# Performance work log

Measured on AMD Instinct MI355X. Metric: run time of the kernel, lower is better.

## Reference

```python
import jax, jax.numpy as jnp
import numpy as np

BN_EPS = 1e-5

def _conv1x1(x, w, b):
    # x: [B,C,H,W], w: [O,C], b: [O] -> [B,O,H,W]
    return jnp.einsum('bchw,oc->bohw', x, w) + b[None, :, None, None]

def setup_inputs() -> dict:
    key = jax.random.key(0)
    ks = jax.random.split(key, 9)
    B, C, H, W = 8, 256, 64, 64
    I = C // 2
    s_in = 1.0 / np.sqrt(C)
    s_out = 1.0 / np.sqrt(I)
    return {
        'x':       jax.random.normal(ks[0], (B, C, H, W), dtype=jnp.float32),
        'g_w':     jax.random.uniform(ks[1], (I, C), jnp.float32, -s_in, s_in),
        'g_b':     jax.random.uniform(ks[2], (I,),  jnp.float32, -s_in, s_in),
        'theta_w': jax.random.uniform(ks[3], (I, C), jnp.float32, -s_in, s_in),
        'theta_b': jax.random.uniform(ks[4], (I,),  jnp.float32, -s_in, s_in),
        'phi_w':   jax.random.uniform(ks[5], (I, C), jnp.float32, -s_in, s_in),
        'phi_b':   jax.random.uniform(ks[6], (I,),  jnp.float32, -s_in, s_in),
        'w_w':     jax.random.uniform(ks[7], (C, I), jnp.float32, -s_out, s_out),
        'w_b':     jax.random.uniform(ks[8], (C,),  jnp.float32, -s_out, s_out),
        'gamma':   jnp.ones((C,), dtype=jnp.float32),   # BN weight init constant 1
        'beta':    jnp.zeros((C,), dtype=jnp.float32),  # BN bias init constant 0
    }

def reference(x, g_w, g_b, theta_w, theta_b, phi_w, phi_b, w_w, w_b, gamma, beta):
    B, C, H, W = x.shape
    I = g_w.shape[0]
    N = H * W
    g_x     = _conv1x1(x, g_w, g_b).reshape(B, I, N)          # [B,I,N]
    theta_x = _conv1x1(x, theta_w, theta_b).reshape(B, I, N)  # [B,I,N]
    phi_x   = _conv1x1(x, phi_w, phi_b).reshape(B, I, N)      # [B,I,N]
    # f = theta^T @ phi : [B,N,N]
    f = jnp.einsum('bin,bim->bnm', theta_x, phi_x)
    a = jax.nn.softmax(f, axis=-1)
    # y = a @ g^T : [B,N,I] -> [B,I,H,W]
    y = jnp.einsum('bnm,bim->bin', a, g_x).reshape(B, I, H, W)
    wy = _conv1x1(y, w_w, w_b)                                # [B,C,H,W]
    # BatchNorm2d (training mode: batch statistics over B,H,W per channel)
    mean = jnp.mean(wy, axis=(0, 2, 3), keepdims=True)
    var = jnp.var(wy, axis=(0, 2, 3), keepdims=True)
    wy_bn = (wy - mean) * jax.lax.rsqrt(var + BN_EPS)
    wy_bn = wy_bn * gamma[None, :, None, None] + beta[None, :, None, None]
    return wy_bn + x
```

## Files before the change

kernel.cpp:

```cpp
#include <hip/hip_runtime.h>

#define B_ 8
#define C_ 256
#define I_ 128
#define N_ 4096
#define BN_ (B_ * N_)
#define LOG2E 1.4426950408889634f

typedef __attribute__((ext_vector_type(8))) short bf16x8;
typedef __attribute__((ext_vector_type(4))) float f32x4;
typedef __attribute__((ext_vector_type(4))) int i32x4;

static __device__ __forceinline__ short f2bf(float f) {
    unsigned u = __float_as_uint(f);
    unsigned r = u + 0x7fffu + ((u >> 16) & 1u);
    return (short)(r >> 16);
}
static __device__ __forceinline__ float bf2f(short s) {
    return __uint_as_float(((unsigned)(unsigned short)s) << 16);
}
static __device__ __forceinline__ unsigned cvt_pk_bf16(float lo, float hi) {
    unsigned r;
    asm("v_cvt_pk_bf16_f32 %0, %1, %2" : "=v"(r) : "v"(lo), "v"(hi));
    return r;
}

__global__ void k_prep(const float* g_w, const float* theta_w, const float* phi_w,
                       const float* g_b, const float* theta_b, const float* phi_b,
                       const float* w_w, short* wcat, short* wwb, float* bcat) {
    int i = blockIdx.x * 256 + threadIdx.x;
    if (i < 384 * 256) {
        int j = i >> 8, c = i & 255;
        float v = (j < 128) ? theta_w[j * 256 + c] * LOG2E
                : (j < 256) ? phi_w[(j - 128) * 256 + c]
                            : g_w[(j - 256) * 256 + c];
        wcat[i] = f2bf(v);
    } else if (i < 384 * 256 + 256 * 128) {
        int k = i - 384 * 256;
        wwb[k] = f2bf(w_w[k]);
    } else if (i < 384 * 256 + 256 * 128 + 384) {
        int j = i - (384 * 256 + 256 * 128);
        bcat[j] = (j < 128) ? theta_b[j] * LOG2E
                : (j < 256) ? phi_b[j - 128] : g_b[j - 256];
    }
}

__global__ __launch_bounds__(256) void k_proj(const float* __restrict__ x,
                                              const short* __restrict__ wcat,
                                              const float* __restrict__ bcat,
                                              short* __restrict__ tp,
                                              short* __restrict__ gmat) {
    int b = blockIdx.y;
    int n0 = blockIdx.x * 64;
    int tid = threadIdx.x;
    int wave = tid >> 6, lane = tid & 63, s = lane & 15, q = lane >> 4;
    __shared__ short xs[64][264];

#pragma unroll
    for (int it = 0; it < 16; ++it) {
        int cr = (tid >> 4) + it * 16;
        int nc = tid & 15;
        const float4 v = *(const float4*)&x[((size_t)b * C_ + cr) * N_ + n0 + nc * 4];
        xs[nc * 4 + 0][cr] = f2bf(v.x);
        xs[nc * 4 + 1][cr] = f2bf(v.y);
        xs[nc * 4 + 2][cr] = f2bf(v.z);
        xs[nc * 4 + 3][cr] = f2bf(v.w);
    }
    __syncthreads();

    f32x4 acc[4][6];
#pragma unroll
    for (int rt = 0; rt < 4; ++rt)
#pragma unroll
        for (int jt = 0; jt < 6; ++jt) acc[rt][jt] = (f32x4){0.f, 0.f, 0.f, 0.f};

#pragma unroll
    for (int kb = 0; kb < 8; ++kb) {
        bf16x8 af[4], bfv[6];
#pragma unroll
        for (int rt = 0; rt < 4; ++rt)
            af[rt] = *(const bf16x8*)&xs[rt * 16 + s][kb * 32 + q * 8];
#pragma unroll
        for (int jt = 0; jt < 6; ++jt)
            bfv[jt] = *(const bf16x8*)&wcat[(wave * 96 + jt * 16 + s) * 256 + kb * 32 + q * 8];
#pragma unroll
        for (int rt = 0; rt < 4; ++rt)
#pragma unroll
            for (int jt = 0; jt < 6; ++jt)
                acc[rt][jt] = __builtin_amdgcn_mfma_f32_16x16x32_bf16(af[rt], bfv[jt], acc[rt][jt], 0, 0, 0);
    }

#pragma unroll
    for (int rt = 0; rt < 4; ++rt)
#pragma unroll
        for (int jt = 0; jt < 6; ++jt) {
            int j = wave * 96 + jt * 16 + s;
            float bias = bcat[j];
#pragma unroll
            for (int r = 0; r < 4; ++r) {
                int n = n0 + rt * 16 + 4 * q + r;
                float v = acc[rt][jt][r] + bias;
                if (j < 256)
                    tp[((size_t)b * N_ + n) * 256 + j] = f2bf(v);
                else
                    gmat[((size_t)b * I_ + (j - 256)) * N_ + n] = f2bf(v);
            }
        }
}

__global__ __launch_bounds__(512, 2) void k_attn_wy(const short* __restrict__ tp,
                                                    const short* __restrict__ gmat,
                                                    const short* __restrict__ wwb,
                                                    const float* __restrict__ w_b,
                                                    short* __restrict__ wyh) {
    int id = blockIdx.x;
    int b = id & 7;
    int qt = id >> 3;
    int n0 = qt * 128;
    int tid = threadIdx.x;
    int wave = tid >> 6, lane = tid & 63, s = lane & 15, q = lane >> 4;

    __shared__ __align__(16) short SH[65536];
    __shared__ float l_lds[128];
    char* base = (char*)SH;

    const int swz = (s & 7) << 4;
    int kA[4];
#pragma unroll
    for (int kb = 0; kb < 4; ++kb) kA[kb] = s * 256 + ((kb * 64 + q * 16) ^ swz);
    int vA[2];
#pragma unroll
    for (int kb2 = 0; kb2 < 2; ++kb2) vA[kb2] = s * 256 + ((kb2 * 64 + q * 16) ^ swz);
    int krow = tid >> 4, kch = tid & 15;
    int stW = krow * 256 + ((kch * 16) ^ ((krow & 7) << 4));

    bf16x8 qf[4];
    {
        const short* qb = tp + ((size_t)b * N_ + n0 + wave * 16 + s) * 256;
#pragma unroll
        for (int kb = 0; kb < 4; ++kb) qf[kb] = *(const bf16x8*)(qb + kb * 32 + q * 8);
    }

    f32x4 ot[8];
#pragma unroll
    for (int t = 0; t < 8; ++t) ot[t] = (f32x4){0.f, 0.f, 0.f, 0.f};
    float lsum = 0.f;

    bf16x8 pk[4], pv[4];
#pragma unroll
    for (int it = 0; it < 4; ++it) {
        pk[it] = *(const bf16x8*)&tp[((size_t)b * N_ + krow + it * 32) * 256 + 128 + kch * 8];
        pv[it] = *(const bf16x8*)&gmat[((size_t)b * I_ + krow + it * 32) * N_ + kch * 8];
    }
#pragma unroll
    for (int it = 0; it < 4; ++it) {
        *(bf16x8*)(base + stW + it * 8192) = pk[it];
        *(bf16x8*)(base + 32768 + stW + it * 8192) = pv[it];
    }
    __syncthreads();

    for (int i = 0; i < 32; ++i) {
        char* KtB = base + (i & 1) * 65536;
        char* VtB = KtB + 32768;
        if (i < 31) {
            int m = (i + 1) * 128;
#pragma unroll
            for (int it = 0; it < 4; ++it) {
                pk[it] = *(const bf16x8*)&tp[((size_t)b * N_ + m + krow + it * 32) * 256 + 128 + kch * 8];
                pv[it] = *(const bf16x8*)&gmat[((size_t)b * I_ + krow + it * 32) * N_ + m + kch * 8];
            }
        }

#pragma unroll
        for (int h = 0; h < 2; ++h) {
            const int hK = h * 16384, hV = h * 128;

            f32x4 sa[4];
#pragma unroll
            for (int tc = 0; tc < 4; ++tc) sa[tc] = (f32x4){0.f, 0.f, 0.f, 0.f};
            __builtin_amdgcn_s_setprio(1);
#pragma unroll
            for (int tc = 0; tc < 4; ++tc) {
#pragma unroll
                for (int kb = 0; kb < 4; ++kb) {
                    bf16x8 bfv = *(const bf16x8*)(KtB + hK + kA[kb] + tc * 4096);
                    sa[tc] = __builtin_amdgcn_mfma_f32_16x16x32_bf16(bfv, qf[kb], sa[tc], 0, 0, 0);
                }
            }
            __builtin_amdgcn_s_setprio(0);

#pragma unroll
            for (int tc = 0; tc < 4; ++tc)
#pragma unroll
                for (int r = 0; r < 4; ++r) sa[tc][r] = exp2f(sa[tc][r]);
            {
                float t0 = (sa[0][0] + sa[0][1]) + (sa[0][2] + sa[0][3]);
                float t1 = (sa[1][0] + sa[1][1]) + (sa[1][2] + sa[1][3]);
                float t2 = (sa[2][0] + sa[2][1]) + (sa[2][2] + sa[2][3]);
                float t3 = (sa[3][0] + sa[3][1]) + (sa[3][2] + sa[3][3]);
                lsum += (t0 + t1) + (t2 + t3);
            }
            unsigned W[4][2];
#pragma unroll
            for (int tc = 0; tc < 4; ++tc) {
                W[tc][0] = cvt_pk_bf16(sa[tc][0], sa[tc][1]);
                W[tc][1] = cvt_pk_bf16(sa[tc][2], sa[tc][3]);
            }

#pragma unroll
            for (int kb2 = 0; kb2 < 2; ++kb2) {
                unsigned rA = W[2 * kb2 + 0][0];
                unsigned rB = W[2 * kb2 + 0][1];
                unsigned rC = W[2 * kb2 + 1][0];
                unsigned rD = W[2 * kb2 + 1][1];
                asm("v_permlane32_swap_b32 %0, %1" : "+v"(rA), "+v"(rC));
                asm("v_permlane32_swap_b32 %0, %1" : "+v"(rB), "+v"(rD));
                asm("v_permlane16_swap_b32 %0, %1" : "+v"(rA), "+v"(rC));
                asm("v_permlane16_swap_b32 %0, %1" : "+v"(rB), "+v"(rD));
                i32x4 wv = (i32x4){(int)rA, (int)rB, (int)rC, (int)rD};
                bf16x8 pa = __builtin_bit_cast(bf16x8, wv);
                __builtin_amdgcn_s_setprio(1);
#pragma unroll
                for (int t = 0; t < 8; ++t) {
                    bf16x8 vb = *(const bf16x8*)(VtB + hV + vA[kb2] + t * 4096);
                    ot[t] = __builtin_amdgcn_mfma_f32_16x16x32_bf16(pa, vb, ot[t], 0, 0, 0);
                }
                __builtin_amdgcn_s_setprio(0);
            }
        }

        if (i < 31) {
            char* KtN = base + ((i & 1) ^ 1) * 65536;
#pragma unroll
            for (int it = 0; it < 4; ++it) {
                *(bf16x8*)(KtN + stW + it * 8192) = pk[it];
                *(bf16x8*)(KtN + 32768 + stW + it * 8192) = pv[it];
            }
        }
        __syncthreads();
    }

    lsum += __shfl_xor(lsum, 16);
    lsum += __shfl_xor(lsum, 32);
    if (lane < 16) l_lds[wave * 16 + s] = lsum;

#pragma unroll
    for (int t = 0; t < 8; ++t)
#pragma unroll
        for (int r = 0; r < 4; ++r) {
            int row = wave * 16 + 4 * q + r;
            int byt = row * 256 + (((t * 16 + s) * 2) ^ ((row & 7) << 4));
            *(short*)(base + byt) = f2bf(ot[t][r]);
        }
    __syncthreads();

    f32x4 acc[2][8];
#pragma unroll
    for (int ct = 0; ct < 2; ++ct)
#pragma unroll
        for (int jt = 0; jt < 8; ++jt) acc[ct][jt] = (f32x4){0.f, 0.f, 0.f, 0.f};
#pragma unroll
    for (int kb = 0; kb < 4; ++kb) {
        bf16x8 af[2];
#pragma unroll
        for (int ct = 0; ct < 2; ++ct)
            af[ct] = *(const bf16x8*)&wwb[(wave * 32 + ct * 16 + s) * 128 + kb * 32 + q * 8];
#pragma unroll
        for (int jt = 0; jt < 8; ++jt) {
            bf16x8 yb = *(const bf16x8*)(base + kA[kb] + jt * 4096);
#pragma unroll
            for (int ct = 0; ct < 2; ++ct)
                acc[ct][jt] = __builtin_amdgcn_mfma_f32_16x16x32_bf16(af[ct], yb, acc[ct][jt], 0, 0, 0);
        }
    }
    float linv[8];
#pragma unroll
    for (int jt = 0; jt < 8; ++jt) linv[jt] = 1.0f / l_lds[jt * 16 + s];
#pragma unroll
    for (int ct = 0; ct < 2; ++ct)
#pragma unroll
        for (int r = 0; r < 4; ++r) {
            int c = wave * 32 + ct * 16 + 4 * q + r;
            float bias = w_b[c];
#pragma unroll
            for (int jt = 0; jt < 8; ++jt)
                wyh[((size_t)b * C_ + c) * N_ + n0 + jt * 16 + s] =
                    f2bf(acc[ct][jt][r] * linv[jt] + bias);
        }
}

__global__ __launch_bounds__(256) void k_stats(const short* __restrict__ wyh,
                                               const float* __restrict__ gamma,
                                               const float* __restrict__ beta,
                                               float* __restrict__ scale,
                                               float* __restrict__ shift) {
    int c = blockIdx.x;
    int tid = threadIdx.x;
    float s1 = 0.f, s2 = 0.f;
    for (int b = 0; b < B_; ++b) {
        const short* p = wyh + ((size_t)b * C_ + c) * N_;
        for (int idx = tid * 8; idx < N_; idx += 2048) {
            bf16x8 v = *(const bf16x8*)&p[idx];
#pragma unroll
            for (int j = 0; j < 8; ++j) {
                float f = bf2f(v[j]);
                s1 += f;
                s2 += f * f;
            }
        }
    }
#pragma unroll
    for (int off = 1; off < 64; off <<= 1) {
        s1 += __shfl_xor(s1, off);
        s2 += __shfl_xor(s2, off);
    }
    __shared__ float r1[4], r2[4];
    if ((tid & 63) == 0) { r1[tid >> 6] = s1; r2[tid >> 6] = s2; }
    __syncthreads();
    if (tid == 0) {
        float t1 = r1[0] + r1[1] + r1[2] + r1[3];
        float t2 = r2[0] + r2[1] + r2[2] + r2[3];
        const float inv = 1.0f / 32768.0f;
        float mean = t1 * inv;
        float var = t2 * inv - mean * mean;
        float sc = gamma[c] * rsqrtf(var + 1e-5f);
        scale[c] = sc;
        shift[c] = beta[c] - mean * sc;
    }
}

__global__ __launch_bounds__(256) void k_out(const short* __restrict__ wyh,
                                             const float* __restrict__ x,
                                             const float* __restrict__ scale,
                                             const float* __restrict__ shift,
                                             float* __restrict__ out) {
    int gid = blockIdx.x * 256 + threadIdx.x;
    size_t base = (size_t)gid * 8;
    int c = (int)((base >> 12) & 255);
    float sc = scale[c], sh = shift[c];
    bf16x8 w = *(const bf16x8*)&wyh[base];
    float4 x0 = *(const float4*)&x[base];
    float4 x1 = *(const float4*)&x[base + 4];
    float4 o0, o1;
    o0.x = bf2f(w[0]) * sc + sh + x0.x;
    o0.y = bf2f(w[1]) * sc + sh + x0.y;
    o0.z = bf2f(w[2]) * sc + sh + x0.z;
    o0.w = bf2f(w[3]) * sc + sh + x0.w;
    o1.x = bf2f(w[4]) * sc + sh + x1.x;
    o1.y = bf2f(w[5]) * sc + sh + x1.y;
    o1.z = bf2f(w[6]) * sc + sh + x1.z;
    o1.w = bf2f(w[7]) * sc + sh + x1.w;
    *(float4*)&out[base] = o0;
    *(float4*)&out[base + 4] = o1;
}

extern "C" void kernel_launch(void* const* d_in, const int* in_sizes, int n_in,
                              void* d_out, int out_size, void* d_ws, size_t ws_size,
                              hipStream_t stream) {
    const float* x       = (const float*)d_in[0];
    const float* g_w     = (const float*)d_in[1];
    const float* g_b     = (const float*)d_in[2];
    const float* theta_w = (const float*)d_in[3];
    const float* theta_b = (const float*)d_in[4];
    const float* phi_w   = (const float*)d_in[5];
    const float* phi_b   = (const float*)d_in[6];
    const float* w_w     = (const float*)d_in[7];
    const float* w_b     = (const float*)d_in[8];
    const float* gamma   = (const float*)d_in[9];
    const float* beta    = (const float*)d_in[10];

    char* ws = (char*)d_ws;
    size_t off = 0;
    auto alloc = [&](size_t bytes) {
        void* p = ws + off;
        off += (bytes + 255) & ~(size_t)255;
        return p;
    };
    short*  wcat  = (short*)alloc((size_t)384 * 256 * 2);
    short*  wwb   = (short*)alloc((size_t)256 * 128 * 2);
    float*  bcat  = (float*)alloc((size_t)384 * 4);
    float*  scale = (float*)alloc(256 * 4);
    float*  shift = (float*)alloc(256 * 4);
    short*  tp    = (short*)alloc((size_t)BN_ * 256 * 2);
    short*  gmat  = (short*)alloc((size_t)B_ * I_ * N_ * 2);
    short*  wyh   = (short*)alloc((size_t)BN_ * C_ * 2);

    k_prep<<<514, 256, 0, stream>>>(g_w, theta_w, phi_w, g_b, theta_b, phi_b, w_w,
                                    wcat, wwb, bcat);
    k_proj<<<dim3(64, 8), 256, 0, stream>>>(x, wcat, bcat, tp, gmat);
    k_attn_wy<<<256, 512, 0, stream>>>(tp, gmat, wwb, w_b, wyh);
    k_stats<<<256, 256, 0, stream>>>(wyh, gamma, beta, scale, shift);
    k_out<<<4096, 256, 0, stream>>>(wyh, x, scale, shift, (float*)d_out);
}
```

Baseline: 236.4 us.

## Split KV halves across wave groups with two query fragments per wave

```diff
diff --git a/kernel.cpp b/kernel.cpp
--- a/kernel.cpp
+++ b/kernel.cpp
@@ -119,9 +119,10 @@
     int n0 = qt * 128;
     int tid = threadIdx.x;
     int wave = tid >> 6, lane = tid & 63, s = lane & 15, q = lane >> 4;
+    int kg = wave >> 2, qg = wave & 3;
 
     __shared__ __align__(16) short SH[65536];
-    __shared__ float l_lds[128];
+    __shared__ float l_lds[2][128];
     char* base = (char*)SH;
 
     const int swz = (s & 7) << 4;
@@ -134,17 +135,23 @@
     int krow = tid >> 4, kch = tid & 15;
     int stW = krow * 256 + ((kch * 16) ^ ((krow & 7) << 4));
 
-    bf16x8 qf[4];
-    {
-        const short* qb = tp + ((size_t)b * N_ + n0 + wave * 16 + s) * 256;
-#pragma unroll
-        for (int kb = 0; kb < 4; ++kb) qf[kb] = *(const bf16x8*)(qb + kb * 32 + q * 8);
-    }
-
-    f32x4 ot[8];
-#pragma unroll
-    for (int t = 0; t < 8; ++t) ot[t] = (f32x4){0.f, 0.f, 0.f, 0.f};
-    float lsum = 0.f;
+    i32x4 onesw = (i32x4){0x3F803F80, 0x3F803F80, 0x3F803F80, 0x3F803F80};
+    bf16x8 vone = __builtin_bit_cast(bf16x8, onesw);
+
+    bf16x8 qf[2][4];
+#pragma unroll
+    for (int fr = 0; fr < 2; ++fr) {
+        const short* qb = tp + ((size_t)b * N_ + n0 + qg * 32 + fr * 16 + s) * 256;
+#pragma unroll
+        for (int kb = 0; kb < 4; ++kb) qf[fr][kb] = *(const bf16x8*)(qb + kb * 32 + q * 8);
+    }
+
+    f32x4 ot[2][8];
+#pragma unroll
+    for (int fr = 0; fr < 2; ++fr)
+#pragma unroll
+        for (int t = 0; t < 8; ++t) ot[fr][t] = (f32x4){0.f, 0.f, 0.f, 0.f};
+    f32x4 lacc[2] = {(f32x4){0.f, 0.f, 0.f, 0.f}, (f32x4){0.f, 0.f, 0.f, 0.f}};
 
     bf16x8 pk[4], pv[4];
 #pragma unroll
@@ -158,6 +165,8 @@
         *(bf16x8*)(base + 32768 + stW + it * 8192) = pv[it];
     }
     __syncthreads();
+
+    const int hK = kg * 16384, hV = kg * 128;
 
     for (int i = 0; i < 32; ++i) {
         char* KtB = base + (i & 1) * 65536;
@@ -171,62 +180,66 @@
             }
         }
 
-#pragma unroll
-        for (int h = 0; h < 2; ++h) {
-            const int hK = h * 16384, hV = h * 128;
-
-            f32x4 sa[4];
-#pragma unroll
-            for (int tc = 0; tc < 4; ++tc) sa[tc] = (f32x4){0.f, 0.f, 0.f, 0.f};
-            __builtin_amdgcn_s_setprio(1);
+        f32x4 sa[2][4];
+#pragma unroll
+        for (int fr = 0; fr < 2; ++fr)
+#pragma unroll
+            for (int tc = 0; tc < 4; ++tc) sa[fr][tc] = (f32x4){0.f, 0.f, 0.f, 0.f};
+        __builtin_amdgcn_s_setprio(1);
+#pragma unroll
+        for (int tc = 0; tc < 4; ++tc) {
+            bf16x8 bfv[4];
+#pragma unroll
+            for (int kb = 0; kb < 4; ++kb)
+                bfv[kb] = *(const bf16x8*)(KtB + hK + kA[kb] + tc * 4096);
+#pragma unroll
+            for (int fr = 0; fr < 2; ++fr)
+#pragma unroll
+                for (int kb = 0; kb < 4; ++kb)
+                    sa[fr][tc] = __builtin_amdgcn_mfma_f32_16x16x32_bf16(bfv[kb], qf[fr][kb], sa[fr][tc], 0, 0, 0);
+        }
+        __builtin_amdgcn_s_setprio(0);
+
+        unsigned W[2][4][2];
+#pragma unroll
+        for (int fr = 0; fr < 2; ++fr) {
+#pragma unroll
+            for (int tc = 0; tc < 4; ++tc)
+#pragma unroll
+                for (int r = 0; r < 4; ++r) sa[fr][tc][r] = exp2f(sa[fr][tc][r]);
 #pragma unroll
             for (int tc = 0; tc < 4; ++tc) {
-#pragma unroll
-                for (int kb = 0; kb < 4; ++kb) {
-                    bf16x8 bfv = *(const bf16x8*)(KtB + hK + kA[kb] + tc * 4096);
-                    sa[tc] = __builtin_amdgcn_mfma_f32_16x16x32_bf16(bfv, qf[kb], sa[tc], 0, 0, 0);
-                }
-            }
-            __builtin_amdgcn_s_setprio(0);
-
-#pragma unroll
-            for (int tc = 0; tc < 4; ++tc)
-#pragma unroll
-                for (int r = 0; r < 4; ++r) sa[tc][r] = exp2f(sa[tc][r]);
-            {
-                float t0 = (sa[0][0] + sa[0][1]) + (sa[0][2] + sa[0][3]);
-                float t1 = (sa[1][0] + sa[1][1]) + (sa[1][2] + sa[1][3]);
-                float t2 = (sa[2][0] + sa[2][1]) + (sa[2][2] + sa[2][3]);
-                float t3 = (sa[3][0] + sa[3][1]) + (sa[3][2] + sa[3][3]);
-                lsum += (t0 + t1) + (t2 + t3);
-            }
-            unsigned W[4][2];
-#pragma unroll
-            for (int tc = 0; tc < 4; ++tc) {
-                W[tc][0] = cvt_pk_bf16(sa[tc][0], sa[tc][1]);
-                W[tc][1] = cvt_pk_bf16(sa[tc][2], sa[tc][3]);
-            }
-
-#pragma unroll
-            for (int kb2 = 0; kb2 < 2; ++kb2) {
-                unsigned rA = W[2 * kb2 + 0][0];
-                unsigned rB = W[2 * kb2 + 0][1];
-                unsigned rC = W[2 * kb2 + 1][0];
-                unsigned rD = W[2 * kb2 + 1][1];
+                W[fr][tc][0] = cvt_pk_bf16(sa[fr][tc][0], sa[fr][tc][1]);
+                W[fr][tc][1] = cvt_pk_bf16(sa[fr][tc][2], sa[fr][tc][3]);
+            }
+        }
+
+#pragma unroll
+        for (int kb2 = 0; kb2 < 2; ++kb2) {
+            bf16x8 pa[2];
+#pragma unroll
+            for (int fr = 0; fr < 2; ++fr) {
+                unsigned rA = W[fr][2 * kb2 + 0][0];
+                unsigned rB = W[fr][2 * kb2 + 0][1];
+                unsigned rC = W[fr][2 * kb2 + 1][0];
+                unsigned rD = W[fr][2 * kb2 + 1][1];
                 asm("v_permlane32_swap_b32 %0, %1" : "+v"(rA), "+v"(rC));
                 asm("v_permlane32_swap_b32 %0, %1" : "+v"(rB), "+v"(rD));
                 asm("v_permlane16_swap_b32 %0, %1" : "+v"(rA), "+v"(rC));
                 asm("v_permlane16_swap_b32 %0, %1" : "+v"(rB), "+v"(rD));
                 i32x4 wv = (i32x4){(int)rA, (int)rB, (int)rC, (int)rD};
-                bf16x8 pa = __builtin_bit_cast(bf16x8, wv);
-                __builtin_amdgcn_s_setprio(1);
-#pragma unroll
-                for (int t = 0; t < 8; ++t) {
-                    bf16x8 vb = *(const bf16x8*)(VtB + hV + vA[kb2] + t * 4096);
-                    ot[t] = __builtin_amdgcn_mfma_f32_16x16x32_bf16(pa, vb, ot[t], 0, 0, 0);
-                }
-                __builtin_amdgcn_s_setprio(0);
-            }
+                pa[fr] = __builtin_bit_cast(bf16x8, wv);
+            }
+            __builtin_amdgcn_s_setprio(1);
+            lacc[0] = __builtin_amdgcn_mfma_f32_16x16x32_bf16(pa[0], vone, lacc[0], 0, 0, 0);
+            lacc[1] = __builtin_amdgcn_mfma_f32_16x16x32_bf16(pa[1], vone, lacc[1], 0, 0, 0);
+#pragma unroll
+            for (int t = 0; t < 8; ++t) {
+                bf16x8 vb = *(const bf16x8*)(VtB + hV + vA[kb2] + t * 4096);
+                ot[0][t] = __builtin_amdgcn_mfma_f32_16x16x32_bf16(pa[0], vb, ot[0][t], 0, 0, 0);
+                ot[1][t] = __builtin_amdgcn_mfma_f32_16x16x32_bf16(pa[1], vb, ot[1][t], 0, 0, 0);
+            }
+            __builtin_amdgcn_s_setprio(0);
         }
 
         if (i < 31) {
@@ -240,18 +253,41 @@
         __syncthreads();
     }
 
-    lsum += __shfl_xor(lsum, 16);
-    lsum += __shfl_xor(lsum, 32);
-    if (lane < 16) l_lds[wave * 16 + s] = lsum;
-
-#pragma unroll
-    for (int t = 0; t < 8; ++t)
-#pragma unroll
-        for (int r = 0; r < 4; ++r) {
-            int row = wave * 16 + 4 * q + r;
-            int byt = row * 256 + (((t * 16 + s) * 2) ^ ((row & 7) << 4));
-            *(short*)(base + byt) = f2bf(ot[t][r]);
-        }
+    if (s == 0) {
+#pragma unroll
+        for (int fr = 0; fr < 2; ++fr)
+#pragma unroll
+            for (int r = 0; r < 4; ++r)
+                l_lds[kg][qg * 32 + fr * 16 + 4 * q + r] = lacc[fr][r];
+    }
+    if (kg == 1) {
+#pragma unroll
+        for (int fr = 0; fr < 2; ++fr)
+#pragma unroll
+            for (int t = 0; t < 8; ++t)
+#pragma unroll
+                for (int r = 0; r < 4; ++r) {
+                    int row = qg * 32 + fr * 16 + 4 * q + r;
+                    int colb = (t * 16 + s) * 4;
+                    *(float*)(base + row * 512 + (colb ^ ((row & 7) << 4))) = ot[fr][t][r];
+                }
+    }
+    __syncthreads();
+    if (kg == 0) {
+#pragma unroll
+        for (int fr = 0; fr < 2; ++fr)
+#pragma unroll
+            for (int t = 0; t < 8; ++t)
+#pragma unroll
+                for (int r = 0; r < 4; ++r) {
+                    int row = qg * 32 + fr * 16 + 4 * q + r;
+                    int colb = (t * 16 + s) * 4;
+                    float p = *(const float*)(base + row * 512 + (colb ^ ((row & 7) << 4)));
+                    float v = ot[fr][t][r] + p;
+                    int byt = 65536 + row * 256 + (((t * 16 + s) * 2) ^ ((row & 7) << 4));
+                    *(short*)(base + byt) = f2bf(v);
+                }
+    }
     __syncthreads();
 
     f32x4 acc[2][8];
@@ -267,7 +303,7 @@
             af[ct] = *(const bf16x8*)&wwb[(wave * 32 + ct * 16 + s) * 128 + kb * 32 + q * 8];
 #pragma unroll
         for (int jt = 0; jt < 8; ++jt) {
-            bf16x8 yb = *(const bf16x8*)(base + kA[kb] + jt * 4096);
+            bf16x8 yb = *(const bf16x8*)(base + 65536 + kA[kb] + jt * 4096);
 #pragma unroll
             for (int ct = 0; ct < 2; ++ct)
                 acc[ct][jt] = __builtin_amdgcn_mfma_f32_16x16x32_bf16(af[ct], yb, acc[ct][jt], 0, 0, 0);
@@ -275,7 +311,8 @@
     }
     float linv[8];
 #pragma unroll
-    for (int jt = 0; jt < 8; ++jt) linv[jt] = 1.0f / l_lds[jt * 16 + s];
+    for (int jt = 0; jt < 8; ++jt)
+        linv[jt] = 1.0f / (l_lds[0][jt * 16 + s] + l_lds[1][jt * 16 + s]);
 #pragma unroll
     for (int ct = 0; ct < 2; ++ct)
 #pragma unroll
```

New measurement: 227.2 us. 1.04x faster.
